# Performance work log

Hardware: AMD Instinct MI355X
Metric: run time of the kernel (lower is better)

Reference implementation:

```python
import jax, jax.numpy as jnp
import numpy as np

B, H, K, D = 8192, 8, 4096, 1024
HD = D // H  # head_dim = 128


def _l2norm(x, axis=-1, eps=1e-12):
    n = jnp.linalg.norm(x, axis=axis, keepdims=True)
    return x / jnp.maximum(n, eps)


def setup_inputs() -> dict:
    key = jax.random.key(0)
    kz, kc = jax.random.split(key)
    z = jax.random.normal(kz, (B, D), dtype=jnp.float32)
    # codebooks initialized as in _init_diverse_codebook: randn then L2-normalized per code
    codebooks = _l2norm(jax.random.normal(kc, (H, K, HD), dtype=jnp.float32), axis=2)
    return {"z": z, "codebooks": codebooks}


def reference(z, codebooks):
    bsz, dim = z.shape
    z_r = z.reshape(bsz, H, HD)                      # [B,H,d]
    z_n = _l2norm(z_r, axis=2)
    cb_n = _l2norm(codebooks, axis=2)                # [H,K,d]
    sims = jnp.einsum('bhd,hkd->bhk', z_n, cb_n)     # [B,H,K]
    distances = 1.0 - sims
    indices = jnp.argmax(sims, axis=-1)              # [B,H] int
    # per-head codebook gather, fully vectorized (replaces python loop over heads)
    z_q = codebooks[jnp.arange(H)[None, :], indices]  # [B,H,d]
    # straight-through estimator
    z_q = z_r + jax.lax.stop_gradient(z_q - z_r)
    return (z_q.reshape(bsz, dim), indices, distances)
```

## Files before the change

### kernel.cpp

```cpp
#include <hip/hip_runtime.h>
#include <cstdint>
#include <cstddef>

#define B_SZ 8192
#define H_N  8
#define K_N  4096
#define D_N  1024
#define HD_N 128

typedef __attribute__((ext_vector_type(8))) short bf16x8;
typedef __attribute__((ext_vector_type(4))) float f32x4;

#define GLOAD16(gp, lp)                                                        \
    __builtin_amdgcn_global_load_lds(                                          \
        (const __attribute__((address_space(1))) void*)(gp),                   \
        (__attribute__((address_space(3))) void*)(lp), 16, 0, 0)

__device__ __forceinline__ unsigned int ordf(float f) {
    unsigned int u = __float_as_uint(f);
    return (u & 0x80000000u) ? ~u : (u | 0x80000000u);
}

__device__ __forceinline__ unsigned long long shfl_xor_u64(unsigned long long v, int m) {
    int lo = (int)(unsigned int)v;
    int hi = (int)(unsigned int)(v >> 32);
    lo = __shfl_xor(lo, m, 64);
    hi = __shfl_xor(hi, m, 64);
    return ((unsigned long long)(unsigned int)hi << 32) | (unsigned int)lo;
}

__device__ __forceinline__ unsigned short f2bf(float f) {
    unsigned int u = __float_as_uint(f);
    u += 0x7FFFu + ((u >> 16) & 1u);
    return (unsigned short)(u >> 16);
}
__device__ __forceinline__ float bf2f(unsigned short s) {
    return __uint_as_float((unsigned int)s << 16);
}

template<int ZMODE>
__global__ void normsplit_kernel(const float* __restrict__ in,
                                 unsigned short* __restrict__ out, int nrows) {
    int wid  = (int)((blockIdx.x * blockDim.x + threadIdx.x) >> 6);
    int lane = threadIdx.x & 63;
    if (wid >= nrows) return;
    const float* r;
    size_t orow;
    if (ZMODE) {
        int b = wid >> 3, h = wid & 7;
        r = in + (size_t)b * D_N + h * HD_N;
        orow = (size_t)h * B_SZ + b;
    } else {
        r = in + (size_t)wid * HD_N;
        orow = (size_t)wid;
    }
    float2 v = *(const float2*)(r + lane * 2);
    float ss = v.x * v.x + v.y * v.y;
#pragma unroll
    for (int m = 32; m; m >>= 1) ss += __shfl_xor(ss, m, 64);
    float d = fmaxf(sqrtf(ss), 1e-12f);
    float q0 = v.x / d, q1 = v.y / d;
    unsigned short h0 = f2bf(q0), h1 = f2bf(q1);
    float l0 = q0 - bf2f(h0), l1 = q1 - bf2f(h1);
    unsigned short* op = out + orow * 256;
    *(unsigned int*)(op + lane * 2) =
        (unsigned int)h0 | ((unsigned int)h1 << 16);
    *(unsigned int*)(op + 128 + lane * 2) =
        (unsigned int)f2bf(l0) | ((unsigned int)f2bf(l1) << 16);
}

__global__ __launch_bounds__(256)
void sims_mfma_kernel(const unsigned short* __restrict__ zs,
                      const unsigned short* __restrict__ cs,
                      float* __restrict__ dist,
                      unsigned long long* __restrict__ packed) {
    __shared__ __align__(16) unsigned short As[8][128][8];
    __shared__ __align__(16) unsigned short Bs[8][128][8];

    const int bm = blockIdx.x, bn = blockIdx.y, h = blockIdx.z;
    const int t    = threadIdx.x;
    const int lane = t & 63;
    const int wid  = t >> 6;
    const int wm = wid >> 1, wn = wid & 1;
    const int cl = lane & 15, rg = lane >> 4;

    const unsigned short* Ag = zs + ((size_t)h * B_SZ + (size_t)bm * 128) * 256;
    const unsigned short* Bg = cs + ((size_t)h * K_N  + (size_t)bn * 128) * 256;

    f32x4 acc[4][4];
#pragma unroll
    for (int i = 0; i < 4; ++i)
#pragma unroll
        for (int j = 0; j < 4; ++j) acc[i][j] = (f32x4)0.0f;

    for (int ks = 0; ks < 6; ++ks) {
        const int kb   = ks >> 1;
        const int kin  = (ks & 1) * 64;
        const int aoff = (kb == 1 ? 128 : 0) + kin;
        const int boff = (kb == 2 ? 128 : 0) + kin;
#pragma unroll
        for (int i = 0; i < 4; ++i) {
            const int f = t + i * 256;
            const int r = f & 127;
            const int c = f >> 7;
            GLOAD16(Ag + (size_t)r * 256 + aoff + c * 8, &As[0][0][0] + (size_t)f * 8);
            GLOAD16(Bg + (size_t)r * 256 + boff + c * 8, &Bs[0][0][0] + (size_t)f * 8);
        }
        __syncthreads();

#pragma unroll
        for (int kk = 0; kk < 2; ++kk) {
            const int q = kk * 4 + rg;
            bf16x8 a[4], b[4];
#pragma unroll
            for (int mi = 0; mi < 4; ++mi)
                a[mi] = *(const bf16x8*)&As[q][wm * 64 + mi * 16 + cl][0];
#pragma unroll
            for (int ni = 0; ni < 4; ++ni)
                b[ni] = *(const bf16x8*)&Bs[q][wn * 64 + ni * 16 + cl][0];
#pragma unroll
            for (int mi = 0; mi < 4; ++mi)
#pragma unroll
                for (int ni = 0; ni < 4; ++ni)
                    acc[mi][ni] = __builtin_amdgcn_mfma_f32_16x16x32_bf16(
                        a[mi], b[ni], acc[mi][ni], 0, 0, 0);
        }
        __syncthreads();
    }

#pragma unroll
    for (int mi = 0; mi < 4; ++mi) {
#pragma unroll
        for (int j = 0; j < 4; ++j) {
            const int m = bm * 128 + wm * 64 + mi * 16 + rg * 4 + j;
            const size_t drow = ((size_t)m * H_N + h) * (size_t)K_N
                              + (size_t)bn * 128 + wn * 64;
            unsigned long long best = 0ull;
#pragma unroll
            for (int ni = 0; ni < 4; ++ni) {
                const float s = acc[mi][ni][j];
                dist[drow + ni * 16 + cl] = 1.0f - s;
                const int n = bn * 128 + wn * 64 + ni * 16 + cl;
                unsigned long long p =
                    ((unsigned long long)ordf(s) << 32) |
                    (unsigned int)(K_N - 1 - n);
                best = (p > best) ? p : best;
            }
#pragma unroll
            for (int ml = 1; ml < 16; ml <<= 1) {
                unsigned long long o = shfl_xor_u64(best, ml);
                best = (o > best) ? o : best;
            }
            if (cl == 0) {
                atomicMax(packed + (size_t)m * H_N + h, best);
            }
        }
    }
}

__global__ void finalize_kernel(const unsigned long long* __restrict__ packed,
                                const float* __restrict__ z,
                                const float* __restrict__ cb,
                                float* __restrict__ zq,
                                float* __restrict__ idx_out) {
    int rid  = (int)((blockIdx.x * blockDim.x + threadIdx.x) >> 6);
    int lane = threadIdx.x & 63;
    if (rid >= B_SZ * H_N) return;
    int b = rid >> 3;
    int h = rid & 7;
    unsigned long long p = packed[rid];
    int idx = K_N - 1 - (int)(unsigned int)(p & 0xFFFFFFFFull);
    if (lane == 0) idx_out[rid] = (float)idx;
    const float* crow = cb + ((size_t)h * K_N + idx) * HD_N;
    const float* zrow = z + (size_t)b * D_N + h * HD_N;
    float2 c  = *(const float2*)(crow + lane * 2);
    float2 zr = *(const float2*)(zrow + lane * 2);
    float2 o;
    o.x = zr.x + (c.x - zr.x);
    o.y = zr.y + (c.y - zr.y);
    *(float2*)(zq + (size_t)b * D_N + h * HD_N + lane * 2) = o;
}

extern "C" void kernel_launch(void* const* d_in, const int* in_sizes, int n_in,
                              void* d_out, int out_size, void* d_ws, size_t ws_size,
                              hipStream_t stream) {
    const float* z  = (const float*)d_in[0];
    const float* cb = (const float*)d_in[1];

    float* out  = (float*)d_out;
    float* zq   = out;
    float* idxo = out + (size_t)B_SZ * D_N;
    float* dist = idxo + (size_t)B_SZ * H_N;

    unsigned short* zs = (unsigned short*)d_ws;
    unsigned short* cs = zs + (size_t)H_N * B_SZ * 256;
    unsigned long long* packed =
        (unsigned long long*)(cs + (size_t)H_N * K_N * 256);

    hipMemsetAsync(packed, 0, (size_t)B_SZ * H_N * sizeof(unsigned long long), stream);

    normsplit_kernel<1><<<(B_SZ * H_N) / 4, 256, 0, stream>>>(z, zs, B_SZ * H_N);
    normsplit_kernel<0><<<(H_N * K_N) / 4, 256, 0, stream>>>(cb, cs, H_N * K_N);

    dim3 g(B_SZ / 128, K_N / 128, H_N);
    sims_mfma_kernel<<<g, 256, 0, stream>>>(zs, cs, dist, packed);

    finalize_kernel<<<(B_SZ * H_N) / 4, 256, 0, stream>>>(packed, z, cb, zq, idxo);
}
```

Measured before the change: 1.614 ms.

## Double-buffer LDS tiles to overlap global loads with MFMA compute

The sims kernel now uses two LDS buffers per operand and issues the async global-to-LDS loads for the next k-step before computing on the current one. A single waitcnt-plus-barrier per iteration replaces the two __syncthreads. The aim is to hide global load latency behind MFMA work. In exchange, LDS use doubles, which could lower occupancy. The kernel is likely dominated by writing the large distance output, so the gain may be limited.

```diff
diff --git a/kernel.cpp b/kernel.cpp
--- a/kernel.cpp
+++ b/kernel.cpp
@@ -74,8 +74,8 @@
                       const unsigned short* __restrict__ cs,
                       float* __restrict__ dist,
                       unsigned long long* __restrict__ packed) {
-    __shared__ __align__(16) unsigned short As[8][128][8];
-    __shared__ __align__(16) unsigned short Bs[8][128][8];
+    __shared__ __align__(16) unsigned short As[2][8192];
+    __shared__ __align__(16) unsigned short Bs[2][8192];
 
     const int bm = blockIdx.x, bn = blockIdx.y, h = blockIdx.z;
     const int t    = threadIdx.x;
@@ -93,20 +93,29 @@
 #pragma unroll
         for (int j = 0; j < 4; ++j) acc[i][j] = (f32x4)0.0f;
 
-    for (int ks = 0; ks < 6; ++ks) {
-        const int kb   = ks >> 1;
-        const int kin  = (ks & 1) * 64;
-        const int aoff = (kb == 1 ? 128 : 0) + kin;
-        const int boff = (kb == 2 ? 128 : 0) + kin;
+    const int aoffs[6] = {0, 64, 128, 192, 0, 64};
+    const int boffs[6] = {0, 64, 0, 64, 128, 192};
+
+    auto stage = [&](int buf, int ks) {
+        const int ao = aoffs[ks], bo = boffs[ks];
 #pragma unroll
         for (int i = 0; i < 4; ++i) {
             const int f = t + i * 256;
             const int r = f & 127;
             const int c = f >> 7;
-            GLOAD16(Ag + (size_t)r * 256 + aoff + c * 8, &As[0][0][0] + (size_t)f * 8);
-            GLOAD16(Bg + (size_t)r * 256 + boff + c * 8, &Bs[0][0][0] + (size_t)f * 8);
-        }
-        __syncthreads();
+            GLOAD16(Ag + (size_t)r * 256 + ao + c * 8, &As[buf][f * 8]);
+            GLOAD16(Bg + (size_t)r * 256 + bo + c * 8, &Bs[buf][f * 8]);
+        }
+    };
+
+    stage(0, 0);
+    asm volatile("s_waitcnt vmcnt(0)" ::: "memory");
+    __builtin_amdgcn_s_barrier();
+
+#pragma unroll
+    for (int ks = 0; ks < 6; ++ks) {
+        const int cur = ks & 1;
+        if (ks < 5) stage(cur ^ 1, ks + 1);
 
 #pragma unroll
         for (int kk = 0; kk < 2; ++kk) {
@@ -114,10 +123,10 @@
             bf16x8 a[4], b[4];
 #pragma unroll
             for (int mi = 0; mi < 4; ++mi)
-                a[mi] = *(const bf16x8*)&As[q][wm * 64 + mi * 16 + cl][0];
+                a[mi] = *(const bf16x8*)&As[cur][(q * 128 + wm * 64 + mi * 16 + cl) * 8];
 #pragma unroll
             for (int ni = 0; ni < 4; ++ni)
-                b[ni] = *(const bf16x8*)&Bs[q][wn * 64 + ni * 16 + cl][0];
+                b[ni] = *(const bf16x8*)&Bs[cur][(q * 128 + wn * 64 + ni * 16 + cl) * 8];
 #pragma unroll
             for (int mi = 0; mi < 4; ++mi)
 #pragma unroll
@@ -125,7 +134,11 @@
                     acc[mi][ni] = __builtin_amdgcn_mfma_f32_16x16x32_bf16(
                         a[mi], b[ni], acc[mi][ni], 0, 0, 0);
         }
-        __syncthreads();
+
+        if (ks < 5) {
+            asm volatile("s_waitcnt vmcnt(0)" ::: "memory");
+            __builtin_amdgcn_s_barrier();
+        }
     }
 
 #pragma unroll
```

Result: no change. 1.600 ms (-0.8%).
